# Optimization experiments

Hardware: AMD Instinct MI355X
Metric: run time of the kernel (lower is better)

## Reference

```python
import jax, jax.numpy as jnp
import numpy as np

N_NODES = 50000
N_EDGES = 1600000
IN_FEAT = 128
HIDDEN = 128
NUM_CLASSES = 10
NUM_GRAPHS = 128


def setup_inputs() -> dict:
    key = jax.random.key(0)
    ks = jax.random.split(key, 10)
    x = jax.random.normal(ks[0], (N_NODES, IN_FEAT), dtype=jnp.float32)
    edge_index = jax.random.randint(ks[1], (2, N_EDGES), 0, N_NODES, dtype=jnp.int64)
    batch = jnp.sort(jax.random.randint(ks[2], (N_NODES,), 0, NUM_GRAPHS, dtype=jnp.int64))
    edge_mask = jax.random.uniform(ks[3], (N_EDGES,), dtype=jnp.float32)
    # Glorot-ish init for weights, zeros for biases (PyG default: glorot W, zero bias)
    def glorot(k, fan_in, fan_out):
        s = jnp.sqrt(6.0 / (fan_in + fan_out))
        return jax.random.uniform(k, (fan_in, fan_out), minval=-s, maxval=s, dtype=jnp.float32)
    W1 = glorot(ks[4], IN_FEAT, HIDDEN)
    b1 = jnp.zeros((HIDDEN,), dtype=jnp.float32)
    W2 = glorot(ks[5], HIDDEN, HIDDEN)
    b2 = jnp.zeros((HIDDEN,), dtype=jnp.float32)
    Wfc = glorot(ks[6], HIDDEN, NUM_CLASSES)
    bfc = jnp.zeros((NUM_CLASSES,), dtype=jnp.float32)
    return {"x": x, "edge_index": edge_index, "batch": batch, "edge_mask": edge_mask,
            "W1": W1, "b1": b1, "W2": W2, "b2": b2, "Wfc": Wfc, "bfc": bfc}


def _gcn_conv(x, W, b, edge_index, edge_weight, n_nodes):
    """PyG GCNConv: add self-loops (weight 1), symmetric deg^{-1/2} normalization,
    linear transform, gather-scatter aggregation source->target."""
    row, col = edge_index[0], edge_index[1]
    loop = jnp.arange(n_nodes, dtype=row.dtype)
    row = jnp.concatenate([row, loop])
    col = jnp.concatenate([col, loop])
    ew = jnp.concatenate([edge_weight, jnp.ones((n_nodes,), dtype=edge_weight.dtype)])
    deg = jax.ops.segment_sum(ew, col, num_segments=n_nodes)  # in-degree w.r.t. targets
    dinv = jnp.where(deg > 0, jax.lax.rsqrt(deg), 0.0)
    norm = dinv[row] * ew * dinv[col]                          # [E+N]
    h = x @ W                                                  # [N, out]
    msg = h[row] * norm[:, None]                               # gather + scale
    out = jax.ops.segment_sum(msg, col, num_segments=n_nodes)  # scatter-add
    return out + b


def reference(x, edge_index, batch, edge_mask, W1, b1, W2, b2, Wfc, bfc):
    n = x.shape[0]
    h = jax.nn.relu(_gcn_conv(x, W1, b1, edge_index, edge_mask, n))
    # dropout is identity in eval mode
    h = jax.nn.relu(_gcn_conv(h, W2, b2, edge_index, edge_mask, n))
    pooled = jax.ops.segment_sum(h, batch, num_segments=NUM_GRAPHS)  # global_add_pool
    logits = pooled @ Wfc + bfc
    return jax.nn.log_softmax(logits, axis=1)
```

## Files before the change

### kernel.cpp

```cpp
#include <hip/hip_runtime.h>
#include <hip/hip_bf16.h>

#define NN 50000
#define NE 1600000
#define FEAT 128
#define NG 128
#define NC 10
#define CPAD 16

constexpr int SCAN_BLOCKS = (NN + 255) / 256;

typedef unsigned int u32x4 __attribute__((ext_vector_type(4)));
typedef short bf16x8 __attribute__((ext_vector_type(8)));
typedef float f32x4 __attribute__((ext_vector_type(4)));

__device__ __forceinline__ float bflo(unsigned u) { return __uint_as_float(u << 16); }
__device__ __forceinline__ float bfhi(unsigned u) { return __uint_as_float(u & 0xffff0000u); }
__device__ __forceinline__ float bfs(unsigned short u) { return __uint_as_float(((unsigned)u) << 16); }
__device__ __forceinline__ unsigned packbf(float a, float b) {
    unsigned ua = __float_as_uint(a), ub = __float_as_uint(b);
    ua += 0x7fffu + ((ua >> 16) & 1u);
    ub += 0x7fffu + ((ub >> 16) & 1u);
    return (ua >> 16) | (ub & 0xffff0000u);
}
__device__ __forceinline__ unsigned short bf1(float a) {
    unsigned ua = __float_as_uint(a);
    ua += 0x7fffu + ((ua >> 16) & 1u);
    return (unsigned short)(ua >> 16);
}

__global__ void k_rank(const int* __restrict__ col, int* __restrict__ counts,
                       int* __restrict__ rank) {
    int e = blockIdx.x * blockDim.x + threadIdx.x;
    if (e < NE) rank[e] = atomicAdd(&counts[(size_t)col[e] * CPAD], 1);
}

__global__ void k_scanA(const int* __restrict__ counts, int* __restrict__ offsets,
                        int* __restrict__ blockSums) {
    __shared__ int tmp[256];
    int i = blockIdx.x * 256 + threadIdx.x;
    int v = (i < NN) ? counts[(size_t)i * CPAD] : 0;
    tmp[threadIdx.x] = v;
    __syncthreads();
    for (int off = 1; off < 256; off <<= 1) {
        int t = (threadIdx.x >= off) ? tmp[threadIdx.x - off] : 0;
        __syncthreads();
        tmp[threadIdx.x] += t;
        __syncthreads();
    }
    if (i < NN) offsets[i] = tmp[threadIdx.x] - v;
    if (threadIdx.x == 255) blockSums[blockIdx.x] = tmp[255];
}

__global__ void k_scanB(int* __restrict__ blockSums) {
    __shared__ int tmp[256];
    int t = threadIdx.x;
    int v = (t < SCAN_BLOCKS) ? blockSums[t] : 0;
    tmp[t] = v;
    __syncthreads();
    for (int off = 1; off < 256; off <<= 1) {
        int u = (t >= off) ? tmp[t - off] : 0;
        __syncthreads();
        tmp[t] += u;
        __syncthreads();
    }
    if (t < SCAN_BLOCKS) blockSums[t] = tmp[t] - v;
}

__global__ void k_scanC(int* __restrict__ offsets, const int* __restrict__ blockSums) {
    int i = blockIdx.x * 256 + threadIdx.x;
    if (i < NN) offsets[i] += blockSums[blockIdx.x];
    if (i == 0) offsets[NN] = NE;
}

__global__ void k_fill(const int* __restrict__ row, const int* __restrict__ col,
                       const float* __restrict__ ew, const int* __restrict__ rank,
                       const int* __restrict__ offsets, long long* __restrict__ csr) {
    int e = blockIdx.x * blockDim.x + threadIdx.x;
    if (e < NE) {
        int pos = offsets[col[e]] + rank[e];
        long long v = (long long)(unsigned)row[e] | ((long long)__float_as_int(ew[e]) << 32);
        csr[pos] = v;
    }
}

__global__ void k_dinv2(const int* __restrict__ offsets, const long long* __restrict__ csr,
                        float* __restrict__ dinv) {
    int n = blockIdx.x * blockDim.x + threadIdx.x;
    if (n >= NN) return;
    int s = offsets[n], e = offsets[n + 1];
    float d = 0.f;
    for (int j = s; j < e; ++j)
        d += __int_as_float((int)(csr[j] >> 32));
    dinv[n] = rsqrtf(d + 1.0f);
}

__global__ void k_prepW(const float* __restrict__ W, unsigned short* __restrict__ Wt) {
    int idx = blockIdx.x * 256 + threadIdx.x;
    int k = idx >> 7, n = idx & 127;
    Wt[n * 128 + k] = bf1(W[idx]);
}

template <typename TIN>
__global__ __launch_bounds__(256) void k_gemm_mfma(const TIN* __restrict__ A,
                                                   const unsigned short* __restrict__ Wt,
                                                   const float* __restrict__ dinv,
                                                   unsigned short* __restrict__ C) {
    const int t = threadIdx.x;
    const int wid = t >> 6;
    const int lane = t & 63;
    const int row0 = blockIdx.x * 64 + wid * 16;
    const int l15 = lane & 15;
    const int kg = lane >> 4;

    int arow = row0 + l15;
    if (arow >= NN) arow = NN - 1;
    bf16x8 a[4];
    if constexpr (sizeof(TIN) == 2) {
        const unsigned short* ap = (const unsigned short*)A + (size_t)arow * 128 + kg * 8;
#pragma unroll
        for (int ks = 0; ks < 4; ++ks)
            a[ks] = *(const bf16x8*)(ap + ks * 32);
    } else {
        const float* ap = (const float*)A + (size_t)arow * 128 + kg * 8;
#pragma unroll
        for (int ks = 0; ks < 4; ++ks) {
            float4 v0 = *(const float4*)(ap + ks * 32);
            float4 v1 = *(const float4*)(ap + ks * 32 + 4);
            u32x4 o;
            o.x = packbf(v0.x, v0.y); o.y = packbf(v0.z, v0.w);
            o.z = packbf(v1.x, v1.y); o.w = packbf(v1.z, v1.w);
            a[ks] = __builtin_bit_cast(bf16x8, o);
        }
    }

    f32x4 acc[8];
#pragma unroll
    for (int ct = 0; ct < 8; ++ct) acc[ct] = (f32x4){0.f, 0.f, 0.f, 0.f};

#pragma unroll
    for (int ct = 0; ct < 8; ++ct) {
        const unsigned short* bp = Wt + (size_t)(ct * 16 + l15) * 128 + kg * 8;
#pragma unroll
        for (int ks = 0; ks < 4; ++ks) {
            bf16x8 b = *(const bf16x8*)(bp + ks * 32);
            acc[ct] = __builtin_amdgcn_mfma_f32_16x16x32_bf16(a[ks], b, acc[ct], 0, 0, 0);
        }
    }

    const int drow0 = row0 + kg * 4;
    float di[4];
#pragma unroll
    for (int r = 0; r < 4; ++r)
        di[r] = (drow0 + r < NN) ? dinv[drow0 + r] : 0.f;
#pragma unroll
    for (int ct = 0; ct < 8; ++ct) {
#pragma unroll
        for (int r = 0; r < 4; ++r) {
            int grow = drow0 + r;
            if (grow < NN)
                C[(size_t)grow * 128 + ct * 16 + l15] = bf1(acc[ct][r] * di[r]);
        }
    }
}

__global__ __launch_bounds__(256) void k_agg(const unsigned short* __restrict__ hs,
                                             const int* __restrict__ offsets,
                                             const long long* __restrict__ csr,
                                             const float* __restrict__ dinv,
                                             const float* __restrict__ bias,
                                             unsigned short* __restrict__ outb) {
    const int node = blockIdx.x * 4 + (threadIdx.x >> 6);
    if (node >= NN) return;
    const int lane = threadIdx.x & 63;
    const int qg = lane >> 4;
    const int fl = lane & 15;

    const int start = offsets[node];
    const int cnt = offsets[node + 1] - start;
    const long long* ep = csr + start;
    const uint4* hb = (const uint4*)hs;

    float a0 = 0.f, a1 = 0.f, a2 = 0.f, a3 = 0.f;
    float a4 = 0.f, a5 = 0.f, a6 = 0.f, a7 = 0.f;

    auto fma8 = [&](uint4 v, float w) {
        a0 += bflo(v.x) * w; a1 += bfhi(v.x) * w;
        a2 += bflo(v.y) * w; a3 += bfhi(v.y) * w;
        a4 += bflo(v.z) * w; a5 += bfhi(v.z) * w;
        a6 += bflo(v.w) * w; a7 += bfhi(v.w) * w;
    };

    const int n16 = cnt >> 4;
    for (int i = 0; i < n16; ++i) {
        const int base = i * 16 + qg;
        long long l0 = __builtin_nontemporal_load(ep + base);
        long long l1 = __builtin_nontemporal_load(ep + base + 4);
        long long l2 = __builtin_nontemporal_load(ep + base + 8);
        long long l3 = __builtin_nontemporal_load(ep + base + 12);
        uint4 v0 = hb[(size_t)(int)l0 * 16 + fl];
        uint4 v1 = hb[(size_t)(int)l1 * 16 + fl];
        uint4 v2 = hb[(size_t)(int)l2 * 16 + fl];
        uint4 v3 = hb[(size_t)(int)l3 * 16 + fl];
        fma8(v0, __int_as_float((int)(l0 >> 32)));
        fma8(v1, __int_as_float((int)(l1 >> 32)));
        fma8(v2, __int_as_float((int)(l2 >> 32)));
        fma8(v3, __int_as_float((int)(l3 >> 32)));
    }
    for (int jj = n16 * 16; jj < cnt; jj += 4) {
        int idx = jj + qg;
        bool valid = idx < cnt;
        long long l = __builtin_nontemporal_load(ep + (valid ? idx : cnt - 1));
        float w = valid ? __int_as_float((int)(l >> 32)) : 0.f;
        uint4 v = hb[(size_t)(int)l * 16 + fl];
        fma8(v, w);
    }

    a0 += __shfl_xor(a0, 16); a0 += __shfl_xor(a0, 32);
    a1 += __shfl_xor(a1, 16); a1 += __shfl_xor(a1, 32);
    a2 += __shfl_xor(a2, 16); a2 += __shfl_xor(a2, 32);
    a3 += __shfl_xor(a3, 16); a3 += __shfl_xor(a3, 32);
    a4 += __shfl_xor(a4, 16); a4 += __shfl_xor(a4, 32);
    a5 += __shfl_xor(a5, 16); a5 += __shfl_xor(a5, 32);
    a6 += __shfl_xor(a6, 16); a6 += __shfl_xor(a6, 32);
    a7 += __shfl_xor(a7, 16); a7 += __shfl_xor(a7, 32);

    if (qg == 0) {
        uint4 sv = hb[(size_t)node * 16 + fl];
        fma8(sv, 1.0f);
        float di = dinv[node];
        float4 b0 = *(const float4*)(bias + fl * 8);
        float4 b1 = *(const float4*)(bias + fl * 8 + 4);
        a0 = fmaxf(di * a0 + b0.x, 0.f);
        a1 = fmaxf(di * a1 + b0.y, 0.f);
        a2 = fmaxf(di * a2 + b0.z, 0.f);
        a3 = fmaxf(di * a3 + b0.w, 0.f);
        a4 = fmaxf(di * a4 + b1.x, 0.f);
        a5 = fmaxf(di * a5 + b1.y, 0.f);
        a6 = fmaxf(di * a6 + b1.z, 0.f);
        a7 = fmaxf(di * a7 + b1.w, 0.f);
        u32x4 o;
        o.x = packbf(a0, a1); o.y = packbf(a2, a3);
        o.z = packbf(a4, a5); o.w = packbf(a6, a7);
        __builtin_nontemporal_store(o, (u32x4*)(outb + (size_t)node * 128 + fl * 8));
    }
}

__global__ __launch_bounds__(256) void k_pool(const unsigned short* __restrict__ h3,
                                              const int* __restrict__ batch,
                                              float* __restrict__ pooled) {
    __shared__ float sm[256];
    const int g = blockIdx.x;
    const int f = threadIdx.x & 127;
    const int half = threadIdx.x >> 7;
    int lo = 0, hi = NN;
    while (lo < hi) { int m = (lo + hi) >> 1; if (batch[m] < g) lo = m + 1; else hi = m; }
    int s0 = lo;
    hi = NN;
    while (lo < hi) { int m = (lo + hi) >> 1; if (batch[m] < g + 1) lo = m + 1; else hi = m; }
    int e0 = lo;

    float s = 0.f;
    int n = s0 + half;
    for (; n + 8 <= e0; n += 8) {
        s += bfs(h3[(size_t)n * 128 + f]);
        s += bfs(h3[(size_t)(n + 2) * 128 + f]);
        s += bfs(h3[(size_t)(n + 4) * 128 + f]);
        s += bfs(h3[(size_t)(n + 6) * 128 + f]);
    }
    for (; n < e0; n += 2) s += bfs(h3[(size_t)n * 128 + f]);

    sm[threadIdx.x] = s;
    __syncthreads();
    if (half == 0) pooled[(size_t)g * 128 + f] = sm[threadIdx.x] + sm[threadIdx.x + 128];
}

__global__ __launch_bounds__(64) void k_fc(const float* __restrict__ pooled,
                                           const float* __restrict__ Wfc,
                                           const float* __restrict__ bfc,
                                           float* __restrict__ out) {
    const int g = blockIdx.x;
    const int lane = threadIdx.x;
    float p0 = pooled[(size_t)g * 128 + lane];
    float p1 = pooled[(size_t)g * 128 + 64 + lane];
    float logits[NC];
#pragma unroll
    for (int c = 0; c < NC; ++c) {
        float v = p0 * Wfc[lane * NC + c] + p1 * Wfc[(64 + lane) * NC + c];
#pragma unroll
        for (int off = 32; off > 0; off >>= 1) v += __shfl_down(v, off);
        logits[c] = v;
    }
    if (lane == 0) {
        float mx = -1e30f;
#pragma unroll
        for (int c = 0; c < NC; ++c) { logits[c] += bfc[c]; mx = fmaxf(mx, logits[c]); }
        float s = 0.f;
#pragma unroll
        for (int c = 0; c < NC; ++c) s += expf(logits[c] - mx);
        float lse = mx + logf(s);
#pragma unroll
        for (int c = 0; c < NC; ++c) out[(size_t)g * NC + c] = logits[c] - lse;
    }
}

extern "C" void kernel_launch(void* const* d_in, const int* in_sizes, int n_in,
                              void* d_out, int out_size, void* d_ws, size_t ws_size,
                              hipStream_t stream) {
    const float* x         = (const float*)d_in[0];
    const int*   edge_index= (const int*)d_in[1];
    const int*   batch     = (const int*)d_in[2];
    const float* edge_mask = (const float*)d_in[3];
    const float* W1        = (const float*)d_in[4];
    const float* b1        = (const float*)d_in[5];
    const float* W2        = (const float*)d_in[6];
    const float* b2        = (const float*)d_in[7];
    const float* Wfc       = (const float*)d_in[8];
    const float* bfc       = (const float*)d_in[9];
    float* out = (float*)d_out;

    const int* row = edge_index;
    const int* col = edge_index + NE;

    char* ws = (char*)d_ws;
    size_t off = 0;
    auto alloc = [&](size_t bytes) -> void* {
        off = (off + 255) & ~(size_t)255;
        void* p = ws + off;
        off += bytes;
        return p;
    };
    int*   counts   = (int*)  alloc((size_t)NN * CPAD * 4);
    int*   offsets  = (int*)  alloc((size_t)(NN + 1) * 4);
    int*   blockSums= (int*)  alloc(256 * 4);
    float* dinv     = (float*)alloc((size_t)NN * 4);
    int*   rank     = (int*)  alloc((size_t)NE * 4);
    long long* csr  = (long long*)alloc((size_t)NE * 8);
    unsigned short* hs1 = (unsigned short*)alloc((size_t)NN * FEAT * 2);
    unsigned short* h2  = (unsigned short*)alloc((size_t)NN * FEAT * 2);
    unsigned short* h3  = (unsigned short*)alloc((size_t)NN * FEAT * 2);
    unsigned short* Wt1 = (unsigned short*)alloc((size_t)FEAT * FEAT * 2);
    unsigned short* Wt2 = (unsigned short*)alloc((size_t)FEAT * FEAT * 2);
    float* pooled   = (float*)alloc((size_t)NG * FEAT * 4);

    hipMemsetAsync(counts, 0, (size_t)NN * CPAD * 4, stream);

    k_rank<<<(NE + 255) / 256, 256, 0, stream>>>(col, counts, rank);
    k_scanA<<<SCAN_BLOCKS, 256, 0, stream>>>(counts, offsets, blockSums);
    k_scanB<<<1, 256, 0, stream>>>(blockSums);
    k_scanC<<<SCAN_BLOCKS, 256, 0, stream>>>(offsets, blockSums);
    k_fill<<<(NE + 255) / 256, 256, 0, stream>>>(row, col, edge_mask, rank, offsets, csr);
    k_dinv2<<<(NN + 255) / 256, 256, 0, stream>>>(offsets, csr, dinv);

    k_prepW<<<64, 256, 0, stream>>>(W1, Wt1);
    k_prepW<<<64, 256, 0, stream>>>(W2, Wt2);

    k_gemm_mfma<float><<<(NN + 63) / 64, 256, 0, stream>>>(x, Wt1, dinv, hs1);
    k_agg<<<(NN + 3) / 4, 256, 0, stream>>>(hs1, offsets, csr, dinv, b1, h2);
    k_gemm_mfma<unsigned short><<<(NN + 63) / 64, 256, 0, stream>>>(h2, Wt2, dinv, hs1);
    k_agg<<<(NN + 3) / 4, 256, 0, stream>>>(hs1, offsets, csr, dinv, b2, h3);
    k_pool<<<NG, 256, 0, stream>>>(h3, batch, pooled);
    k_fc<<<NG, 64, 0, stream>>>(pooled, Wfc, bfc, out);
}
```

Measured before the change: 396.3 us.

## Build CSR with two-pass bucketed counting sort instead of global atomics

Replaces the per-edge global-atomic rank, multi-kernel scan, fill, and degree kernels with a two-level counting sort. Edges are first histogrammed into 256-node buckets using shared-memory atomics, then scattered into bucket bins, then sorted within each bucket into the final CSR. Degree sums and dinv are computed in the same final pass. This removes the contended global atomics, the padded counts memset and the separate degree pass, at the cost of an extra intermediate buffer and a single-block serial scan over the block histograms. Within-node edge order becomes nondeterministic, so floating-point sums may vary slightly between runs.

```diff
diff --git a/kernel.cpp b/kernel.cpp
--- a/kernel.cpp
+++ b/kernel.cpp
@@ -6,9 +6,11 @@
 #define FEAT 128
 #define NG 128
 #define NC 10
-#define CPAD 16
-
-constexpr int SCAN_BLOCKS = (NN + 255) / 256;
+
+#define BUCK 256
+#define NBUCK ((NN + BUCK - 1) / BUCK)
+#define EPB 8192
+#define NBLK1 ((NE + EPB - 1) / EPB)
 
 typedef unsigned int u32x4 __attribute__((ext_vector_type(4)));
 typedef short bf16x8 __attribute__((ext_vector_type(8)));
@@ -29,70 +31,113 @@
     return (unsigned short)(ua >> 16);
 }
 
-__global__ void k_rank(const int* __restrict__ col, int* __restrict__ counts,
-                       int* __restrict__ rank) {
-    int e = blockIdx.x * blockDim.x + threadIdx.x;
-    if (e < NE) rank[e] = atomicAdd(&counts[(size_t)col[e] * CPAD], 1);
-}
-
-__global__ void k_scanA(const int* __restrict__ counts, int* __restrict__ offsets,
-                        int* __restrict__ blockSums) {
+__global__ __launch_bounds__(256) void k_hist(const int* __restrict__ col,
+                                              int* __restrict__ blockHist) {
+    __shared__ int h[BUCK];
+    h[threadIdx.x] = 0;
+    __syncthreads();
+    const int base = blockIdx.x * EPB;
+    const int end = min(base + EPB, NE);
+    for (int e = base + threadIdx.x; e < end; e += 256)
+        atomicAdd(&h[col[e] >> 8], 1);
+    __syncthreads();
+    blockHist[threadIdx.x * NBLK1 + blockIdx.x] = h[threadIdx.x];
+}
+
+__global__ __launch_bounds__(256) void k_scanbk(int* __restrict__ blockHist,
+                                                int* __restrict__ bucketOff,
+                                                int* __restrict__ offsets) {
     __shared__ int tmp[256];
-    int i = blockIdx.x * 256 + threadIdx.x;
-    int v = (i < NN) ? counts[(size_t)i * CPAD] : 0;
-    tmp[threadIdx.x] = v;
-    __syncthreads();
-    for (int off = 1; off < 256; off <<= 1) {
-        int t = (threadIdx.x >= off) ? tmp[threadIdx.x - off] : 0;
-        __syncthreads();
-        tmp[threadIdx.x] += t;
-        __syncthreads();
-    }
-    if (i < NN) offsets[i] = tmp[threadIdx.x] - v;
-    if (threadIdx.x == 255) blockSums[blockIdx.x] = tmp[255];
-}
-
-__global__ void k_scanB(int* __restrict__ blockSums) {
-    __shared__ int tmp[256];
-    int t = threadIdx.x;
-    int v = (t < SCAN_BLOCKS) ? blockSums[t] : 0;
-    tmp[t] = v;
-    __syncthreads();
-    for (int off = 1; off < 256; off <<= 1) {
-        int u = (t >= off) ? tmp[t - off] : 0;
+    const int t = threadIdx.x;
+    int sum = 0;
+    if (t < NBUCK) {
+        for (int blk = 0; blk < NBLK1; ++blk) {
+            int v = blockHist[t * NBLK1 + blk];
+            blockHist[t * NBLK1 + blk] = sum;
+            sum += v;
+        }
+    }
+    tmp[t] = sum;
+    __syncthreads();
+    for (int d = 1; d < 256; d <<= 1) {
+        int u = (t >= d) ? tmp[t - d] : 0;
         __syncthreads();
         tmp[t] += u;
         __syncthreads();
     }
-    if (t < SCAN_BLOCKS) blockSums[t] = tmp[t] - v;
-}
-
-__global__ void k_scanC(int* __restrict__ offsets, const int* __restrict__ blockSums) {
-    int i = blockIdx.x * 256 + threadIdx.x;
-    if (i < NN) offsets[i] += blockSums[blockIdx.x];
-    if (i == 0) offsets[NN] = NE;
-}
-
-__global__ void k_fill(const int* __restrict__ row, const int* __restrict__ col,
-                       const float* __restrict__ ew, const int* __restrict__ rank,
-                       const int* __restrict__ offsets, long long* __restrict__ csr) {
-    int e = blockIdx.x * blockDim.x + threadIdx.x;
-    if (e < NE) {
-        int pos = offsets[col[e]] + rank[e];
-        long long v = (long long)(unsigned)row[e] | ((long long)__float_as_int(ew[e]) << 32);
-        csr[pos] = v;
-    }
-}
-
-__global__ void k_dinv2(const int* __restrict__ offsets, const long long* __restrict__ csr,
-                        float* __restrict__ dinv) {
-    int n = blockIdx.x * blockDim.x + threadIdx.x;
-    if (n >= NN) return;
-    int s = offsets[n], e = offsets[n + 1];
-    float d = 0.f;
-    for (int j = s; j < e; ++j)
-        d += __int_as_float((int)(csr[j] >> 32));
-    dinv[n] = rsqrtf(d + 1.0f);
+    const int excl = tmp[t] - sum;
+    if (t < NBUCK) {
+        bucketOff[t] = excl;
+        for (int blk = 0; blk < NBLK1; ++blk)
+            blockHist[t * NBLK1 + blk] += excl;
+    }
+    if (t == 0) { bucketOff[NBUCK] = NE; offsets[NN] = NE; }
+}
+
+__global__ __launch_bounds__(256) void k_scatter(const int* __restrict__ row,
+                                                 const int* __restrict__ col,
+                                                 const float* __restrict__ ew,
+                                                 const int* __restrict__ blockHist,
+                                                 long long* __restrict__ binned) {
+    __shared__ int cur[BUCK];
+    cur[threadIdx.x] = blockHist[threadIdx.x * NBLK1 + blockIdx.x];
+    __syncthreads();
+    const int base = blockIdx.x * EPB;
+    const int end = min(base + EPB, NE);
+    for (int e = base + threadIdx.x; e < end; e += 256) {
+        int c = col[e];
+        int pos = atomicAdd(&cur[c >> 8], 1);
+        long long v = (long long)(unsigned)(row[e] | ((c & 255) << 16)) |
+                      ((long long)__float_as_int(ew[e]) << 32);
+        binned[pos] = v;
+    }
+}
+
+__global__ __launch_bounds__(256) void k_csr(const long long* __restrict__ binned,
+                                             const int* __restrict__ bucketOff,
+                                             long long* __restrict__ csr,
+                                             int* __restrict__ offsets,
+                                             float* __restrict__ dinv) {
+    __shared__ int cnt[BUCK], off[BUCK], cnt2[BUCK];
+    __shared__ float wsum[BUCK];
+    const int b = blockIdx.x;
+    const int t = threadIdx.x;
+    cnt[t] = 0; cnt2[t] = 0; wsum[t] = 0.f;
+    __syncthreads();
+    const int s = bucketOff[b], e = bucketOff[b + 1];
+    for (int i = s + t; i < e; i += 256) {
+        int lo = (int)binned[i];
+        atomicAdd(&cnt[(lo >> 16) & 255], 1);
+    }
+    __syncthreads();
+    int v0 = cnt[t];
+    off[t] = v0;
+    __syncthreads();
+    for (int d = 1; d < 256; d <<= 1) {
+        int u = (t >= d) ? off[t - d] : 0;
+        __syncthreads();
+        off[t] += u;
+        __syncthreads();
+    }
+    int myoff = off[t] - v0;
+    __syncthreads();
+    off[t] = myoff;
+    __syncthreads();
+    for (int i = s + t; i < e; i += 256) {
+        long long v = binned[i];
+        int lo = (int)v;
+        int c = (lo >> 16) & 255;
+        int r = atomicAdd(&cnt2[c], 1);
+        atomicAdd(&wsum[c], __int_as_float((int)(v >> 32)));
+        csr[s + off[c] + r] = (long long)(unsigned)(lo & 0xFFFF) |
+                              (v & 0xFFFFFFFF00000000LL);
+    }
+    __syncthreads();
+    const int node = b * BUCK + t;
+    if (node < NN) {
+        offsets[node] = s + off[t];
+        dinv[node] = rsqrtf(wsum[t] + 1.0f);
+    }
 }
 
 __global__ void k_prepW(const float* __restrict__ W, unsigned short* __restrict__ Wt) {
@@ -330,11 +375,11 @@
         off += bytes;
         return p;
     };
-    int*   counts   = (int*)  alloc((size_t)NN * CPAD * 4);
+    int*   blockHist= (int*)  alloc((size_t)256 * NBLK1 * 4);
+    int*   bucketOff= (int*)  alloc((size_t)(NBUCK + 1) * 4);
     int*   offsets  = (int*)  alloc((size_t)(NN + 1) * 4);
-    int*   blockSums= (int*)  alloc(256 * 4);
     float* dinv     = (float*)alloc((size_t)NN * 4);
-    int*   rank     = (int*)  alloc((size_t)NE * 4);
+    long long* binned = (long long*)alloc((size_t)NE * 8);
     long long* csr  = (long long*)alloc((size_t)NE * 8);
     unsigned short* hs1 = (unsigned short*)alloc((size_t)NN * FEAT * 2);
     unsigned short* h2  = (unsigned short*)alloc((size_t)NN * FEAT * 2);
@@ -343,14 +388,10 @@
     unsigned short* Wt2 = (unsigned short*)alloc((size_t)FEAT * FEAT * 2);
     float* pooled   = (float*)alloc((size_t)NG * FEAT * 4);
 
-    hipMemsetAsync(counts, 0, (size_t)NN * CPAD * 4, stream);
-
-    k_rank<<<(NE + 255) / 256, 256, 0, stream>>>(col, counts, rank);
-    k_scanA<<<SCAN_BLOCKS, 256, 0, stream>>>(counts, offsets, blockSums);
-    k_scanB<<<1, 256, 0, stream>>>(blockSums);
-    k_scanC<<<SCAN_BLOCKS, 256, 0, stream>>>(offsets, blockSums);
-    k_fill<<<(NE + 255) / 256, 256, 0, stream>>>(row, col, edge_mask, rank, offsets, csr);
-    k_dinv2<<<(NN + 255) / 256, 256, 0, stream>>>(offsets, csr, dinv);
+    k_hist<<<NBLK1, 256, 0, stream>>>(col, blockHist);
+    k_scanbk<<<1, 256, 0, stream>>>(blockHist, bucketOff, offsets);
+    k_scatter<<<NBLK1, 256, 0, stream>>>(row, col, edge_mask, blockHist, binned);
+    k_csr<<<NBUCK, 256, 0, stream>>>(binned, bucketOff, csr, offsets, dinv);
 
     k_prepW<<<64, 256, 0, stream>>>(W1, Wt1);
     k_prepW<<<64, 256, 0, stream>>>(W2, Wt2);
```

New measurement: 371.9 us. -6.1%, faster.
